# Kernel optimization log

Measured on AMD Instinct MI355X. Metric: run time of the kernel, lower is better.

## Reference

```python
import jax, jax.numpy as jnp
import numpy as np

N_HEAD = 16

def setup_inputs() -> dict:
    key = jax.random.key(0)
    k1, k2, k3 = jax.random.split(key, 3)
    B, K, C = 2, 2048, 1024
    x = jax.random.normal(k1, (B, K, C), dtype=jnp.float32)
    W_qkv = jax.random.normal(k2, (C, 3 * C), dtype=jnp.float32) * (1.0 / np.sqrt(C))
    b_qkv = jnp.zeros((3 * C,), dtype=jnp.float32)
    W_proj = jax.random.normal(k3, (C, C), dtype=jnp.float32) * (1.0 / np.sqrt(C))
    b_proj = jnp.zeros((C,), dtype=jnp.float32)
    return {"x": x, "W_qkv": W_qkv, "b_qkv": b_qkv, "W_proj": W_proj, "b_proj": b_proj, "K": K}

def reference(x, W_qkv, b_qkv, W_proj, b_proj, K):
    B, _, C = x.shape
    H = N_HEAD
    Dh = C // H
    qkv = x @ W_qkv + b_qkv                      # [B, K, 3C]
    q, k, v = jnp.split(qkv, 3, axis=-1)
    # [B, H, K, Dh]
    q = q.reshape(B, K, H, Dh).transpose(0, 2, 1, 3)
    k = k.reshape(B, K, H, Dh).transpose(0, 2, 1, 3)
    v = v.reshape(B, K, H, Dh).transpose(0, 2, 1, 3)
    att = jnp.einsum('bhqd,bhkd->bhqk', q, k) / jnp.sqrt(jnp.asarray(Dh, dtype=x.dtype))
    causal = jnp.tril(jnp.ones((K, K), dtype=bool))
    att = jnp.where(causal[None, None], att, jnp.asarray(-jnp.inf, dtype=x.dtype))
    att = jax.nn.softmax(att, axis=-1)
    y = jnp.einsum('bhqk,bhkd->bhqd', att, v)    # [B, H, K, Dh]
    y = y.transpose(0, 2, 1, 3).reshape(B, K, C)
    return y @ W_proj + b_proj
```

## Files before the change

kernel.cpp:

```cpp
#include <hip/hip_runtime.h>
#include <hip/hip_bf16.h>
#include <math.h>

typedef __attribute__((ext_vector_type(8))) short short8;
typedef __attribute__((ext_vector_type(4))) float f32x4;
typedef __attribute__((ext_vector_type(4))) short short4v;
typedef __attribute__((ext_vector_type(2))) int int2v;

static __device__ __forceinline__ short f2bf(float f) {
    __hip_bfloat16 h = __float2bfloat16(f);
    return *reinterpret_cast<short*>(&h);
}
static __device__ __forceinline__ void store_out(float* p, float v) { *p = v; }
static __device__ __forceinline__ void store_out(short* p, float v) { *p = f2bf(v); }

#define GLL16(g, l) __builtin_amdgcn_global_load_lds( \
    (const __attribute__((address_space(1))) void*)(g), \
    (__attribute__((address_space(3))) void*)(l), 16, 0, 0)

#if __has_builtin(__builtin_amdgcn_exp2f)
#define EXP2(x) __builtin_amdgcn_exp2f(x)
#else
#define EXP2(x) exp2f(x)
#endif

#if __has_builtin(__builtin_amdgcn_cvt_pk_bf16_f32)
typedef __attribute__((ext_vector_type(2))) __bf16 bf16x2;
static __device__ __forceinline__ int pack2bf(float a, float b) {
    bf16x2 r = __builtin_amdgcn_cvt_pk_bf16_f32(a, b);
    return __builtin_bit_cast(int, r);
}
#else
static __device__ __forceinline__ int pack2bf(float a, float b) {
    unsigned ua = __builtin_bit_cast(unsigned, a) + 0x8000u;
    unsigned ub = __builtin_bit_cast(unsigned, b) + 0x8000u;
    return (int)((ua >> 16) | (ub & 0xFFFF0000u));
}
#endif

static __device__ __forceinline__ void transpose_cast_tile(
    const float* __restrict__ W, short* __restrict__ Wt, int Kd, int N,
    int bx, int by)
{
    __shared__ float ts[32][33];
    const int c0 = bx * 32, r0 = by * 32;
    const int tx = threadIdx.x & 31, ty = threadIdx.x >> 5;
    #pragma unroll
    for (int e = 0; e < 4; ++e)
        ts[ty + e * 8][tx] = W[(size_t)(r0 + ty + e * 8) * N + c0 + tx];
    __syncthreads();
    #pragma unroll
    for (int e = 0; e < 4; ++e)
        Wt[(size_t)(c0 + ty + e * 8) * Kd + r0 + tx] = f2bf(ts[tx][ty + e * 8]);
}

__global__ __launch_bounds__(256) void prep_kernel(
    const float* __restrict__ x,      short* __restrict__ xb,    int nx,
    const float* __restrict__ W_qkv,  short* __restrict__ Wt1,
    const float* __restrict__ W_proj, short* __restrict__ Wt2,
    int C)
{
    const int nbx = nx / 1024;
    const int nb1 = (3 * C / 32) * (C / 32);
    int bid = blockIdx.x;
    if (bid < nbx) {
        int i = (bid * 256 + threadIdx.x) * 4;
        float4 v = *(const float4*)(x + i);
        short4v o = { f2bf(v.x), f2bf(v.y), f2bf(v.z), f2bf(v.w) };
        *(short4v*)(xb + i) = o;
        return;
    }
    bid -= nbx;
    if (bid < nb1) {
        const int nc = 3 * C / 32;
        transpose_cast_tile(W_qkv, Wt1, C, 3 * C, bid % nc, bid / nc);
        return;
    }
    bid -= nb1;
    {
        const int nc = C / 32;
        transpose_cast_tile(W_proj, Wt2, C, C, bid % nc, bid / nc);
    }
}

__global__ __launch_bounds__(256) void vtrans_kernel(
    const short* __restrict__ qkvb, short* __restrict__ vt, int K, int C)
{
    __shared__ short Vs[64][72];
    const int k0 = blockIdx.x * 64, h = blockIdx.y, b = blockIdx.z;
    const size_t rs = (size_t)3 * C;
    const short* src = qkvb + (size_t)b * K * rs + 2 * C + h * 64;
    const int key = threadIdx.x >> 3, d0 = (threadIdx.x & 7) * 8;
    *(short8*)&Vs[key][d0]      = *(const short8*)(src + (size_t)(k0 + key) * rs + d0);
    *(short8*)&Vs[key + 32][d0] = *(const short8*)(src + (size_t)(k0 + key + 32) * rs + d0);
    __syncthreads();
    const int d = threadIdx.x >> 2, kc = threadIdx.x & 3;
    short* dst = vt + ((size_t)(b * 16 + h) * 64 + d) * K + k0 + kc * 16;
    short8 o0, o1;
    #pragma unroll
    for (int j = 0; j < 8; ++j) { o0[j] = Vs[kc * 16 + j][d]; o1[j] = Vs[kc * 16 + 8 + j][d]; }
    *(short8*)dst = o0;
    *(short8*)(dst + 8) = o1;
}

#define GM 128
#define GN 128
#define GK 32

template <typename OutT>
__global__ __launch_bounds__(256) void gemm_mfma_kernel(
    const short* __restrict__ A, const short* __restrict__ Bt,
    const float* __restrict__ bias, OutT* __restrict__ C,
    int M, int N, int Kd, int qcols, float qscale)
{
    __shared__ __attribute__((aligned(16))) short As[GM * GK];
    __shared__ __attribute__((aligned(16))) short Bs[GN * GK];
    const int tid  = threadIdx.x;
    const int lane = tid & 63, w = tid >> 6;
    const int col  = lane & 15, quad = lane >> 4;
    const int wm = (w & 1) * 64, wn = (w >> 1) * 64;
    const int row0 = blockIdx.y * GM, col0 = blockIdx.x * GN;
    const float sc = (col0 < qcols) ? qscale : 1.f;

    const int sr = tid >> 2, scg = (tid & 3) * 8;
    const short* gA = A  + (size_t)(row0 + sr) * Kd + scg;
    const short* gB = Bt + (size_t)(col0 + sr) * Kd + scg;
    short* lA = As + sr * GK + scg;
    short* lB = Bs + sr * GK + scg;
    const size_t skip = (size_t)64 * Kd;

    f32x4 acc[4][4] = {};
    for (int k0 = 0; k0 < Kd; k0 += GK) {
        __syncthreads();
        GLL16(gA,        lA);
        GLL16(gA + skip, lA + 64 * GK);
        GLL16(gB,        lB);
        GLL16(gB + skip, lB + 64 * GK);
        gA += GK; gB += GK;
        __syncthreads();

        short8 aF[4], bF[4];
        #pragma unroll
        for (int mt = 0; mt < 4; ++mt)
            aF[mt] = *(const short8*)&As[(wm + mt * 16 + col) * GK + quad * 8];
        #pragma unroll
        for (int nt = 0; nt < 4; ++nt)
            bF[nt] = *(const short8*)&Bs[(wn + nt * 16 + col) * GK + quad * 8];
        #pragma unroll
        for (int mt = 0; mt < 4; ++mt)
            #pragma unroll
            for (int nt = 0; nt < 4; ++nt)
                acc[mt][nt] = __builtin_amdgcn_mfma_f32_16x16x32_bf16(aF[mt], bF[nt], acc[mt][nt], 0, 0, 0);
    }

    #pragma unroll
    for (int mt = 0; mt < 4; ++mt)
        #pragma unroll
        for (int i = 0; i < 4; ++i) {
            const size_t r = row0 + wm + mt * 16 + quad * 4 + i;
            #pragma unroll
            for (int nt = 0; nt < 4; ++nt) {
                const int c = col0 + wn + nt * 16 + col;
                store_out(&C[r * N + c], (acc[mt][nt][i] + bias[c]) * sc);
            }
        }
}

#define DH 64

__global__ __launch_bounds__(256, 2) void flash_mfma_kernel(
    const short* __restrict__ qkvb,
    const short* __restrict__ vt,
    short* __restrict__ y,
    int K, int C)
{
    __shared__ __attribute__((aligned(16))) short smem[35840];

    const int tid  = threadIdx.x;
    const int lane = tid & 63, w = tid >> 6;
    const int col  = lane & 15, quad = lane >> 4;

    short* Wreg = smem + w * 8320;
    short* Ptw  = smem + 33280 + w * 640;
    float* Or   = (float*)smem;

    const int cmb = blockIdx.x & 31;
    const int g   = blockIdx.x >> 5;
    const int b   = cmb >> 4, h = cmb & 15;

    short8 bOnes;
    #pragma unroll
    for (int j = 0; j < 8; ++j) bOnes[j] = (col == 0) ? (short)0x3F80 : (short)0;

    const size_t rs = (size_t)3 * C;
    const short* qbase = qkvb + (size_t)b * K * rs + h * DH;
    const short* kbase = qbase + C;
    const short* vbase = vt + (size_t)(b * 16 + h) * DH * K;

    const int krow = (lane >> 3) * 4, koff = (lane & 7) * 8;
    const int vrow = lane >> 2,       voff = (lane & 3) * 8;
    const int loff = lane * 8;

    auto stage = [&](int ci, int buf) {
        const int kc = ci * 32;
        short* Kb = Wreg + buf * 4160;
        short* Vb = Kb + 2080;
        #pragma unroll
        for (int c2 = 0; c2 < 4; ++c2)
            GLL16(kbase + (size_t)(kc + krow + c2) * rs + koff, Kb + c2 * 520 + loff);
        #pragma unroll
        for (int c2 = 0; c2 < 4; ++c2)
            GLL16(vbase + (size_t)(c2 * 16 + vrow) * K + kc + voff, Vb + c2 * 520 + loff);
    };

    auto run = [&](int T) {
        const int t0 = T * 64;
        const int NC = 2 * T + 2;

        short8 aQ[4][2];
        #pragma unroll
        for (int qg = 0; qg < 4; ++qg) {
            const short* qp = qbase + (size_t)(t0 + qg * 16 + col) * rs;
            aQ[qg][0] = *(const short8*)(qp + quad * 8);
            aQ[qg][1] = *(const short8*)(qp + 32 + quad * 8);
        }
        f32x4 O[4][4] = {};
        f32x4 L4[4] = {};

        int ci = w, buf = 0;
        if (ci < NC) stage(ci, 0);
        for (; ci < NC; ci += 4) {
            const int kc = ci * 32;
            const int nci = ci + 4;
            if (nci < NC) {
                stage(nci, buf ^ 1);
                asm volatile("s_waitcnt vmcnt(8)" ::: "memory");
            } else {
                asm volatile("s_waitcnt vmcnt(0)" ::: "memory");
            }
            const short* Kb = Wreg + buf * 4160;
            const short* Vb = Kb + 2080;

            short8 bK[2][2], bV[4];
            #pragma unroll
            for (int nb = 0; nb < 2; ++nb) {
                const int kl = col * 2 + nb;
                const int ka = (kl & 3) * 520 + (kl >> 2) * 64 + quad * 8;
                bK[nb][0] = *(const short8*)&Kb[ka];
                bK[nb][1] = *(const short8*)&Kb[ka + 32];
            }
            #pragma unroll
            for (int db = 0; db < 4; ++db)
                bV[db] = *(const short8*)&Vb[db * 520 + col * 32 + quad * 8];

            #pragma unroll
            for (int qg = 0; qg < 4; ++qg) {
                const int qb = t0 + qg * 16;
                f32x4 S[2] = {};
                #pragma unroll
                for (int nb = 0; nb < 2; ++nb) {
                    S[nb] = __builtin_amdgcn_mfma_f32_16x16x32_bf16(aQ[qg][0], bK[nb][0], S[nb], 0, 0, 0);
                    S[nb] = __builtin_amdgcn_mfma_f32_16x16x32_bf16(aQ[qg][1], bK[nb][1], S[nb], 0, 0, 0);
                }
                if (kc + 31 <= qb) {
                    #pragma unroll
                    for (int i = 0; i < 4; ++i)
                        *(int*)&Ptw[(quad * 4 + i) * 40 + col * 2] =
                            pack2bf(EXP2(S[0][i]), EXP2(S[1][i]));
                } else {
                    const int kg = kc + col * 2;
                    #pragma unroll
                    for (int i = 0; i < 4; ++i) {
                        const int q = qb + quad * 4 + i;
                        float s0 = (kg + 0 <= q) ? S[0][i] : -INFINITY;
                        float s1 = (kg + 1 <= q) ? S[1][i] : -INFINITY;
                        *(int*)&Ptw[(quad * 4 + i) * 40 + col * 2] =
                            pack2bf(EXP2(s0), EXP2(s1));
                    }
                }
                asm volatile("s_waitcnt lgkmcnt(0)" ::: "memory");
                short8 aP = *(const short8*)&Ptw[col * 40 + quad * 8];
                #pragma unroll
                for (int db = 0; db < 4; ++db)
                    O[qg][db] = __builtin_amdgcn_mfma_f32_16x16x32_bf16(aP, bV[db], O[qg][db], 0, 0, 0);
                L4[qg] = __builtin_amdgcn_mfma_f32_16x16x32_bf16(aP, bOnes, L4[qg], 0, 0, 0);
            }
            buf ^= 1;
        }

        __syncthreads();
        for (int ww = 0; ww < 4; ++ww) {
            if (w == ww) {
                #pragma unroll
                for (int qg = 0; qg < 4; ++qg)
                    #pragma unroll
                    for (int i = 0; i < 4; ++i) {
                        const int row = qg * 16 + quad * 4 + i;
                        #pragma unroll
                        for (int db = 0; db < 4; ++db) {
                            float v = O[qg][db][i];
                            if (ww == 0) Or[row * 68 + db * 16 + col] = v;
                            else         Or[row * 68 + db * 16 + col] += v;
                        }
                        if (col == 0) {
                            if (ww == 0) Or[row * 68 + 64] = L4[qg][i];
                            else         Or[row * 68 + 64] += L4[qg][i];
                        }
                    }
            }
            __syncthreads();
        }

        #pragma unroll
        for (int rstep = 0; rstep < 4; ++rstep) {
            const int row = w * 16 + rstep * 4 + quad;
            f32x4 ov = *(const f32x4*)&Or[row * 68 + col * 4];
            const float inv = 1.f / Or[row * 68 + 64];
            int2v o2 = { pack2bf(ov[0] * inv, ov[1] * inv),
                         pack2bf(ov[2] * inv, ov[3] * inv) };
            *(int2v*)(y + ((size_t)b * K + t0 + row) * C + h * DH + col * 4) = o2;
        }
        __syncthreads();
    };

    run(g);
    run(31 - g);
}

extern "C" void kernel_launch(void* const* d_in, const int* in_sizes, int n_in,
                              void* d_out, int out_size, void* d_ws, size_t ws_size,
                              hipStream_t stream)
{
    const float* x      = (const float*)d_in[0];
    const float* W_qkv  = (const float*)d_in[1];
    const float* b_qkv  = (const float*)d_in[2];
    const float* W_proj = (const float*)d_in[3];
    const float* b_proj = (const float*)d_in[4];

    const int B = 2, K = 2048, C = 1024, H = 16;
    const int M = B * K;
    const float C2 = 0.18033688f;

    char* ws = (char*)d_ws;
    short* xb    = (short*)ws;  ws += (size_t)M * C * 2;
    short* Wt1   = (short*)ws;  ws += (size_t)3 * C * C * 2;
    short* Wt2   = (short*)ws;  ws += (size_t)C * C * 2;
    short* qkvb  = (short*)ws;  ws += (size_t)M * 3 * C * 2;
    short* yb    = (short*)ws;  ws += (size_t)M * C * 2;
    short* vtb   = (short*)ws;

    const int nbx = (M * C) / 1024;
    const int nb1 = (3 * C / 32) * (C / 32);
    const int nb2 = (C / 32) * (C / 32);
    prep_kernel<<<nbx + nb1 + nb2, 256, 0, stream>>>(x, xb, M * C, W_qkv, Wt1, W_proj, Wt2, C);

    dim3 g1((3 * C) / GN, M / GM);
    gemm_mfma_kernel<short><<<g1, 256, 0, stream>>>(xb, Wt1, b_qkv, qkvb, M, 3 * C, C, C, C2);

    dim3 gv(K / 64, H, B);
    vtrans_kernel<<<gv, 256, 0, stream>>>(qkvb, vtb, K, C);

    const int NPAIR = (K / 64) / 2;
    flash_mfma_kernel<<<dim3(NPAIR * 32), 256, 0, stream>>>(qkvb, vtb, yb, K, C);

    dim3 g3(C / GN, M / GM);
    gemm_mfma_kernel<float><<<g3, 256, 0, stream>>>(yb, Wt2, b_proj, (float*)d_out, M, C, C, 0, 1.f);
}
```

Before: 197.0 us.

## Drop K/V double buffering, use per-group P tiles, parallelize cross-wave reduction

```diff
diff --git a/kernel.cpp b/kernel.cpp
--- a/kernel.cpp
+++ b/kernel.cpp
@@ -174,15 +174,15 @@
     short* __restrict__ y,
     int K, int C)
 {
-    __shared__ __attribute__((aligned(16))) short smem[35840];
+    __shared__ __attribute__((aligned(16))) short smem[26880];
 
     const int tid  = threadIdx.x;
     const int lane = tid & 63, w = tid >> 6;
     const int col  = lane & 15, quad = lane >> 4;
 
-    short* Wreg = smem + w * 8320;
-    short* Ptw  = smem + 33280 + w * 640;
-    float* Or   = (float*)smem;
+    short* Kb = smem + w * 4160;
+    short* Vb = Kb + 2080;
+    short* Pw = smem + 16640 + w * 2560;
 
     const int cmb = blockIdx.x & 31;
     const int g   = blockIdx.x >> 5;
@@ -201,18 +201,6 @@
     const int vrow = lane >> 2,       voff = (lane & 3) * 8;
     const int loff = lane * 8;
 
-    auto stage = [&](int ci, int buf) {
-        const int kc = ci * 32;
-        short* Kb = Wreg + buf * 4160;
-        short* Vb = Kb + 2080;
-        #pragma unroll
-        for (int c2 = 0; c2 < 4; ++c2)
-            GLL16(kbase + (size_t)(kc + krow + c2) * rs + koff, Kb + c2 * 520 + loff);
-        #pragma unroll
-        for (int c2 = 0; c2 < 4; ++c2)
-            GLL16(vbase + (size_t)(c2 * 16 + vrow) * K + kc + voff, Vb + c2 * 520 + loff);
-    };
-
     auto run = [&](int T) {
         const int t0 = T * 64;
         const int NC = 2 * T + 2;
@@ -227,19 +215,15 @@
         f32x4 O[4][4] = {};
         f32x4 L4[4] = {};
 
-        int ci = w, buf = 0;
-        if (ci < NC) stage(ci, 0);
-        for (; ci < NC; ci += 4) {
+        for (int ci = w; ci < NC; ci += 4) {
             const int kc = ci * 32;
-            const int nci = ci + 4;
-            if (nci < NC) {
-                stage(nci, buf ^ 1);
-                asm volatile("s_waitcnt vmcnt(8)" ::: "memory");
-            } else {
-                asm volatile("s_waitcnt vmcnt(0)" ::: "memory");
-            }
-            const short* Kb = Wreg + buf * 4160;
-            const short* Vb = Kb + 2080;
+            #pragma unroll
+            for (int c2 = 0; c2 < 4; ++c2)
+                GLL16(kbase + (size_t)(kc + krow + c2) * rs + koff, Kb + c2 * 520 + loff);
+            #pragma unroll
+            for (int c2 = 0; c2 < 4; ++c2)
+                GLL16(vbase + (size_t)(c2 * 16 + vrow) * K + kc + voff, Vb + c2 * 520 + loff);
+            asm volatile("s_waitcnt vmcnt(0)" ::: "memory");
 
             short8 bK[2][2], bV[4];
             #pragma unroll
@@ -256,6 +240,7 @@
             #pragma unroll
             for (int qg = 0; qg < 4; ++qg) {
                 const int qb = t0 + qg * 16;
+                short* Ptq = Pw + qg * 640;
                 f32x4 S[2] = {};
                 #pragma unroll
                 for (int nb = 0; nb < 2; ++nb) {
@@ -265,7 +250,7 @@
                 if (kc + 31 <= qb) {
                     #pragma unroll
                     for (int i = 0; i < 4; ++i)
-                        *(int*)&Ptw[(quad * 4 + i) * 40 + col * 2] =
+                        *(int*)&Ptq[(quad * 4 + i) * 40 + col * 2] =
                             pack2bf(EXP2(S[0][i]), EXP2(S[1][i]));
                 } else {
                     const int kg = kc + col * 2;
@@ -274,50 +259,58 @@
                         const int q = qb + quad * 4 + i;
                         float s0 = (kg + 0 <= q) ? S[0][i] : -INFINITY;
                         float s1 = (kg + 1 <= q) ? S[1][i] : -INFINITY;
-                        *(int*)&Ptw[(quad * 4 + i) * 40 + col * 2] =
+                        *(int*)&Ptq[(quad * 4 + i) * 40 + col * 2] =
                             pack2bf(EXP2(s0), EXP2(s1));
                     }
                 }
-                asm volatile("s_waitcnt lgkmcnt(0)" ::: "memory");
-                short8 aP = *(const short8*)&Ptw[col * 40 + quad * 8];
+                short8 aP = *(const short8*)&Ptq[col * 40 + quad * 8];
                 #pragma unroll
                 for (int db = 0; db < 4; ++db)
                     O[qg][db] = __builtin_amdgcn_mfma_f32_16x16x32_bf16(aP, bV[db], O[qg][db], 0, 0, 0);
                 L4[qg] = __builtin_amdgcn_mfma_f32_16x16x32_bf16(aP, bOnes, L4[qg], 0, 0, 0);
             }
-            buf ^= 1;
-        }
-
-        __syncthreads();
-        for (int ww = 0; ww < 4; ++ww) {
-            if (w == ww) {
+        }
+
+        float* OrA = (float*)smem;
+        float* OrB = OrA + 64 * 68;
+        __syncthreads();
+        if (w < 2) {
+            float* R = (w == 0) ? OrA : OrB;
+            #pragma unroll
+            for (int qg = 0; qg < 4; ++qg)
                 #pragma unroll
-                for (int qg = 0; qg < 4; ++qg)
+                for (int i = 0; i < 4; ++i) {
+                    const int row = qg * 16 + quad * 4 + i;
                     #pragma unroll
-                    for (int i = 0; i < 4; ++i) {
-                        const int row = qg * 16 + quad * 4 + i;
-                        #pragma unroll
-                        for (int db = 0; db < 4; ++db) {
-                            float v = O[qg][db][i];
-                            if (ww == 0) Or[row * 68 + db * 16 + col] = v;
-                            else         Or[row * 68 + db * 16 + col] += v;
-                        }
-                        if (col == 0) {
-                            if (ww == 0) Or[row * 68 + 64] = L4[qg][i];
-                            else         Or[row * 68 + 64] += L4[qg][i];
-                        }
-                    }
-            }
-            __syncthreads();
-        }
+                    for (int db = 0; db < 4; ++db)
+                        R[row * 68 + db * 16 + col] = O[qg][db][i];
+                    if (col == 0) R[row * 68 + 64] = L4[qg][i];
+                }
+        }
+        __syncthreads();
+        if (w >= 2) {
+            float* R = (w == 2) ? OrA : OrB;
+            #pragma unroll
+            for (int qg = 0; qg < 4; ++qg)
+                #pragma unroll
+                for (int i = 0; i < 4; ++i) {
+                    const int row = qg * 16 + quad * 4 + i;
+                    #pragma unroll
+                    for (int db = 0; db < 4; ++db)
+                        R[row * 68 + db * 16 + col] += O[qg][db][i];
+                    if (col == 0) R[row * 68 + 64] += L4[qg][i];
+                }
+        }
+        __syncthreads();
 
         #pragma unroll
         for (int rstep = 0; rstep < 4; ++rstep) {
             const int row = w * 16 + rstep * 4 + quad;
-            f32x4 ov = *(const f32x4*)&Or[row * 68 + col * 4];
-            const float inv = 1.f / Or[row * 68 + 64];
-            int2v o2 = { pack2bf(ov[0] * inv, ov[1] * inv),
-                         pack2bf(ov[2] * inv, ov[3] * inv) };
+            f32x4 oa = *(const f32x4*)&OrA[row * 68 + col * 4];
+            f32x4 ob = *(const f32x4*)&OrB[row * 68 + col * 4];
+            const float inv = 1.f / (OrA[row * 68 + 64] + OrB[row * 68 + 64]);
+            int2v o2 = { pack2bf((oa[0] + ob[0]) * inv, (oa[1] + ob[1]) * inv),
+                         pack2bf((oa[2] + ob[2]) * inv, (oa[3] + ob[3]) * inv) };
             *(int2v*)(y + ((size_t)b * K + t0 + row) * C + h * DH + col * 4) = o2;
         }
         __syncthreads();
```

Result: faster. 192.7 us (-2.2%).
